# Kernel tuning notes

Hardware: AMD Instinct MI355X
Metric: run time of the kernel (lower is better)

## Reference

```python
import jax, jax.numpy as jnp
import numpy as np

B, S, D_IN, D_H, D_OUT = 4, 2048, 512, 512, 512


def setup_inputs() -> dict:
    key = jax.random.key(0)
    ks = jax.random.split(key, 11)
    s_in = 1.0 / np.sqrt(D_IN)
    s_cat = 1.0 / np.sqrt(3 * D_H)
    return {
        "x1": jax.random.normal(ks[0], (B, S, D_IN), jnp.float32),
        "x2": jax.random.normal(ks[1], (B, S, D_IN), jnp.float32),
        "x3": jax.random.normal(ks[2], (B, S, D_IN), jnp.float32),
        "Wq": jax.random.normal(ks[3], (D_IN, D_H), jnp.float32) * s_in,
        "bq": jnp.zeros((D_H,), jnp.float32),
        "Wk": jax.random.normal(ks[4], (D_IN, D_H), jnp.float32) * s_in,
        "bk": jnp.zeros((D_H,), jnp.float32),
        "Wv": jax.random.normal(ks[5], (D_IN, D_H), jnp.float32) * s_in,
        "bv": jnp.zeros((D_H,), jnp.float32),
        "Wo": jax.random.normal(ks[6], (3 * D_H, D_OUT), jnp.float32) * s_cat,
        "bo": jnp.zeros((D_OUT,), jnp.float32),
    }


def _attn(Q, K, V):
    # Q: [B,S,H], K/V: [B,S,H] -> [B,S,H]
    scale = 1.0 / jnp.sqrt(jnp.asarray(K.shape[-1], Q.dtype))
    scores = jnp.einsum('bqh,bkh->bqk', Q, K) * scale
    w = jax.nn.softmax(scores, axis=-1)
    return jnp.einsum('bqk,bkh->bqh', w, V)


def reference(x1, x2, x3, Wq, bq, Wk, bk, Wv, bv, Wo, bo):
    Q1, Q2, Q3 = x1 @ Wq + bq, x2 @ Wq + bq, x3 @ Wq + bq
    K1, K2, K3 = x1 @ Wk + bk, x2 @ Wk + bk, x3 @ Wk + bk
    V1, V2, V3 = x1 @ Wv + bv, x2 @ Wv + bv, x3 @ Wv + bv
    fused_x1 = _attn(Q1, K2, V2) + _attn(Q1, K3, V3)
    fused_x2 = _attn(Q2, K1, V1) + _attn(Q2, K3, V3)
    fused_x3 = _attn(Q3, K1, V1) + _attn(Q3, K2, V2)
    fused = jnp.concatenate([fused_x1, fused_x2, fused_x3], axis=-1)
    return fused @ Wo + bo
```

## Files before the change

kernel.cpp:

```cpp
#include <hip/hip_runtime.h>
#include <hip/hip_bf16.h>

typedef __attribute__((ext_vector_type(4))) float  f32x4;
typedef __attribute__((ext_vector_type(8))) short  short8;

#define GAS(p) ((const __attribute__((address_space(1))) void*)(p))
#define LAS(p) ((__attribute__((address_space(3))) void*)(p))

__device__ inline short bf16_of(float f) {
    union { float f; unsigned u; } v; v.f = f;
    unsigned r = v.u + 0x7FFFu + ((v.u >> 16) & 1u);
    return (short)(r >> 16);
}

__device__ __forceinline__ void stage64(const short* A, long lda,
                                        const short* B, long ldb,
                                        short* As, short* Bs) {
    const int tid = threadIdx.x;
    const int w = tid >> 6, l = tid & 63;
    const int r = l >> 3;
    const int scol = ((l & 7) ^ r) * 8;
#pragma unroll
    for (int q = 0; q < 4; ++q) {
        const int rowb = q * 32 + w * 8;
        __builtin_amdgcn_global_load_lds(GAS(A + (long)(rowb + r) * lda + scol),
                                         LAS(As + rowb * 64), 16, 0, 0);
        __builtin_amdgcn_global_load_lds(GAS(B + (long)(rowb + r) * ldb + scol),
                                         LAS(Bs + rowb * 64), 16, 0, 0);
    }
}

__device__ __forceinline__ void gemm_core64(const short* A, long lda,
                                            const short* B, long ldb, int nk,
                                            short* sA, short* sB,
                                            f32x4 acc[4][4]) {
    const int tid = threadIdx.x;
    const int lane = tid & 63, wid = tid >> 6;
    const int wr = wid >> 1, wc = wid & 1;
    const int fr = lane & 15, fk = lane >> 4;
    const int swz = (fr & 7) << 4;
    const int abase = (wr * 64 + fr) * 128 + fk * 16;
    const int bbase = (wc * 64 + fr) * 128 + fk * 16;

    stage64(A, lda, B, ldb, sA, sB);
    __syncthreads();
    for (int ks = 0; ks < nk; ++ks) {
        const int cur = ks & 1;
        if (ks + 1 < nk)
            stage64(A + (ks + 1) * 64, lda, B + (ks + 1) * 64, ldb,
                    sA + (cur ^ 1) * 8192, sB + (cur ^ 1) * 8192);
        const char* pa = (const char*)(sA + cur * 8192);
        const char* pb = (const char*)(sB + cur * 8192);
        short8 af[2][4], bfr[2][4];
#pragma unroll
        for (int kk = 0; kk < 2; ++kk) {
#pragma unroll
            for (int mi = 0; mi < 4; ++mi)
                af[kk][mi] = *(const short8*)(pa + (((abase + kk * 64) ^ swz) + mi * 2048));
#pragma unroll
            for (int ni = 0; ni < 4; ++ni)
                bfr[kk][ni] = *(const short8*)(pb + (((bbase + kk * 64) ^ swz) + ni * 2048));
        }
#pragma unroll
        for (int kk = 0; kk < 2; ++kk)
#pragma unroll
            for (int mi = 0; mi < 4; ++mi)
#pragma unroll
                for (int ni = 0; ni < 4; ++ni)
                    acc[mi][ni] = __builtin_amdgcn_mfma_f32_16x16x32_bf16(af[kk][mi], bfr[kk][ni], acc[mi][ni], 0, 0, 0);
        __syncthreads();
    }
}

__device__ __forceinline__ void bounce_store(short* Pb, const short vals[4][4][4],
                                             short* C, long ldc) {
    const int tid = threadIdx.x, lane = tid & 63, wid = tid >> 6;
    const int wr = wid >> 1, wc = wid & 1, fr = lane & 15, fk = lane >> 4;
#pragma unroll
    for (int mi = 0; mi < 4; ++mi)
#pragma unroll
        for (int ni = 0; ni < 4; ++ni)
#pragma unroll
            for (int r = 0; r < 4; ++r) {
                const int row = wr * 64 + mi * 16 + fk * 4 + r;
                const int col = wc * 64 + ni * 16 + fr;
                Pb[row * 128 + (col ^ ((row & 7) << 3))] = vals[mi][ni][r];
            }
    __syncthreads();
#pragma unroll
    for (int i = 0; i < 8; ++i) {
        const int row = i * 16 + (tid >> 4);
        const int ch = tid & 15;
        short8 v = *(const short8*)&Pb[row * 128 + ((ch * 8) ^ ((row & 7) << 3))];
        *(short8*)&C[(long)row * ldc + ch * 8] = v;
    }
}

__global__ __launch_bounds__(256, 2)
void proj_qk_k(const short* __restrict__ xb, const short* __restrict__ WqkT,
               short* __restrict__ Qb, short* __restrict__ Kb,
               const float* __restrict__ bq, const float* __restrict__ bk) {
    __shared__ short sA[2 * 8192], sB[2 * 8192];
    const short* Ab = xb + (long)blockIdx.x * 128 * 512;
    const short* Bb = WqkT + (long)blockIdx.y * 128 * 512;
    f32x4 acc[4][4] = {};
    gemm_core64(Ab, 512, Bb, 512, 8, sA, sB, acc);

    const int lane = threadIdx.x & 63, wid = threadIdx.x >> 6;
    const int wr = wid >> 1, wc = wid & 1, fr = lane & 15, fk = lane >> 4;
    const int qc0 = blockIdx.y * 128;
    const float* bias = qc0 < 512 ? bq + qc0 : bk + (qc0 - 512);
    short vals[4][4][4];
#pragma unroll
    for (int mi = 0; mi < 4; ++mi)
#pragma unroll
        for (int ni = 0; ni < 4; ++ni) {
            const float bv_ = bias[wc * 64 + ni * 16 + fr];
#pragma unroll
            for (int r = 0; r < 4; ++r)
                vals[mi][ni][r] = bf16_of(acc[mi][ni][r] + bv_);
        }
    short* dst = (qc0 < 512 ? Qb + qc0 : Kb + (qc0 - 512)) + (long)blockIdx.x * 128 * 512;
    bounce_store(sA, vals, dst, 512);
}

__global__ __launch_bounds__(256, 2)
void proj_vt_k(const short* __restrict__ WvT, const short* __restrict__ xb,
               short* __restrict__ VT, const float* __restrict__ bv) {
    __shared__ short sA[2 * 8192], sB[2 * 8192];
    const short* Ab = WvT + (long)blockIdx.x * 128 * 512;
    const short* Bb = xb + (long)blockIdx.y * 128 * 512;
    f32x4 acc[4][4] = {};
    gemm_core64(Ab, 512, Bb, 512, 8, sA, sB, acc);

    const int lane = threadIdx.x & 63, wid = threadIdx.x >> 6;
    const int wr = wid >> 1, wc = wid & 1, fr = lane & 15, fk = lane >> 4;
    short vals[4][4][4];
#pragma unroll
    for (int mi = 0; mi < 4; ++mi)
#pragma unroll
        for (int ni = 0; ni < 4; ++ni)
#pragma unroll
            for (int r = 0; r < 4; ++r) {
                const int rowg = blockIdx.x * 128 + wr * 64 + mi * 16 + fk * 4 + r;
                vals[mi][ni][r] = bf16_of(acc[mi][ni][r] + bv[rowg]);
            }
    bounce_store(sA, vals, VT + (long)blockIdx.x * 128 * 24576 + blockIdx.y * 128, 24576);
}

struct Off6 { long a[6], b[6]; };

__global__ __launch_bounds__(256, 2)
void qk_exp(const short* __restrict__ Qb, const short* __restrict__ Kb,
            short* __restrict__ Sc, float* __restrict__ lpart,
            Off6 o, int z0, float kscale) {
    __shared__ short sA[2 * 8192], sB[2 * 8192];
    const int z = blockIdx.z, slice = z0 + z;
    const int gp = slice >> 2, b = slice & 3;
    const short* Ab = Qb + o.a[gp] + ((long)b * 2048 + (long)blockIdx.x * 128) * 512;
    const short* Bb = Kb + o.b[gp] + ((long)b * 2048 + (long)blockIdx.y * 128) * 512;
    f32x4 acc[4][4] = {};
    gemm_core64(Ab, 512, Bb, 512, 8, sA, sB, acc);

    const int tid = threadIdx.x, lane = tid & 63, wid = tid >> 6;
    const int wr = wid >> 1, wc = wid & 1, fr = lane & 15, fk = lane >> 4;

#pragma unroll
    for (int mi = 0; mi < 4; ++mi)
#pragma unroll
        for (int ni = 0; ni < 4; ++ni)
#pragma unroll
            for (int r = 0; r < 4; ++r)
                acc[mi][ni][r] = exp2f(acc[mi][ni][r] * kscale);

#pragma unroll
    for (int mi = 0; mi < 4; ++mi)
#pragma unroll
        for (int r = 0; r < 4; ++r) {
            float s = acc[mi][0][r] + acc[mi][1][r] + acc[mi][2][r] + acc[mi][3][r];
            s += __shfl_xor(s, 1); s += __shfl_xor(s, 2);
            s += __shfl_xor(s, 4); s += __shfl_xor(s, 8);
            if (fr == 0)
                lpart[((long)z * 32 + blockIdx.y * 2 + wc) * 2048 +
                      (long)blockIdx.x * 128 + wr * 64 + mi * 16 + fk * 4 + r] = s;
        }

    short vals[4][4][4];
#pragma unroll
    for (int mi = 0; mi < 4; ++mi)
#pragma unroll
        for (int ni = 0; ni < 4; ++ni)
#pragma unroll
            for (int r = 0; r < 4; ++r)
                vals[mi][ni][r] = bf16_of(acc[mi][ni][r]);

    short* Cb = Sc + (long)z * 2048 * 2048 +
                (long)blockIdx.x * 128 * 2048 + (long)blockIdx.y * 128;
    bounce_store(sA, vals, Cb, 2048);
}

struct POff { long v[6], c[6]; };

__global__ __launch_bounds__(256, 2)
void pv_div(const short* __restrict__ Sc, const short* __restrict__ VT,
            const float* __restrict__ lpart, short* __restrict__ F,
            POff o, int z0) {
    __shared__ short sA[2 * 8192], sB[2 * 8192];
    const int z = blockIdx.z, slice = z0 + z;
    const int gp = slice >> 2, b = slice & 3;
    const short* Ab = Sc + (long)z * 2048 * 2048 + (long)blockIdx.x * 128 * 2048;
    const short* Bb = VT + o.v[gp] + (long)b * 2048 + (long)blockIdx.y * 128 * 24576;
    f32x4 acc[4][4] = {};
    gemm_core64(Ab, 2048, Bb, 24576, 32, sA, sB, acc);

    const int tid = threadIdx.x, lane = tid & 63, wid = tid >> 6;
    const int wr = wid >> 1, wc = wid & 1, fr = lane & 15, fk = lane >> 4;

    float* linv_s = (float*)sB;
    if (tid < 128) {
        const float* lp = lpart + ((long)z * 32) * 2048 + (long)blockIdx.x * 128 + tid;
        float s = 0.f;
#pragma unroll
        for (int j = 0; j < 32; ++j) s += lp[(long)j * 2048];
        linv_s[tid] = 1.0f / s;
    }
    __syncthreads();

    short vals[4][4][4];
#pragma unroll
    for (int mi = 0; mi < 4; ++mi) {
        float linv[4];
#pragma unroll
        for (int r = 0; r < 4; ++r) linv[r] = linv_s[wr * 64 + mi * 16 + fk * 4 + r];
#pragma unroll
        for (int ni = 0; ni < 4; ++ni)
#pragma unroll
            for (int r = 0; r < 4; ++r)
                vals[mi][ni][r] = bf16_of(acc[mi][ni][r] * linv[r]);
    }
    __syncthreads();

    short* Cb = F + ((long)b * 2048 + (long)blockIdx.x * 128) * 3072 +
                o.c[gp] + (long)blockIdx.y * 128;
    bounce_store(sA, vals, Cb, 3072);
}

__global__ __launch_bounds__(256, 2)
void final_f32(const short* __restrict__ A, const short* __restrict__ B,
               float* __restrict__ C, const float* __restrict__ bias) {
    __shared__ short sA[2 * 8192], sB[2 * 8192];
    const short* Ab = A + (long)blockIdx.x * 128 * 3072;
    const short* Bb = B + (long)blockIdx.y * 128 * 3072;
    f32x4 acc[4][4] = {};
    gemm_core64(Ab, 3072, Bb, 3072, 48, sA, sB, acc);

    const int lane = threadIdx.x & 63, wid = threadIdx.x >> 6;
    const int wr = wid >> 1, wc = wid & 1, fr = lane & 15, fk = lane >> 4;
    const long r0 = (long)blockIdx.x * 128 + wr * 64 + fk * 4;
    const long c0 = (long)blockIdx.y * 128 + wc * 64 + fr;
#pragma unroll
    for (int mi = 0; mi < 4; ++mi)
#pragma unroll
        for (int ni = 0; ni < 4; ++ni) {
            const long rr = r0 + mi * 16, cc = c0 + ni * 16;
#pragma unroll
            for (int r = 0; r < 4; ++r)
                C[(rr + r) * 512 + cc] = acc[mi][ni][r] + bias[cc];
        }
}

__global__ __launch_bounds__(256)
void xconv(const float* __restrict__ x0, const float* __restrict__ x1,
           const float* __restrict__ x2, short* __restrict__ xb) {
    const float* s = blockIdx.z == 0 ? x0 : (blockIdx.z == 1 ? x1 : x2);
    const long i = ((long)blockIdx.x * 256 + threadIdx.x) * 8;
    f32x4 a = *(const f32x4*)(s + i), c = *(const f32x4*)(s + i + 4);
    short8 v;
    v[0] = bf16_of(a.x); v[1] = bf16_of(a.y); v[2] = bf16_of(a.z); v[3] = bf16_of(a.w);
    v[4] = bf16_of(c.x); v[5] = bf16_of(c.y); v[6] = bf16_of(c.z); v[7] = bf16_of(c.w);
    *(short8*)(xb + (long)blockIdx.z * 8192 * 512 + i) = v;
}

__global__ __launch_bounds__(256)
void wprep(const float* __restrict__ Wq, const float* __restrict__ Wk,
           const float* __restrict__ Wv, const float* __restrict__ Wo,
           short* __restrict__ WqkT, short* __restrict__ WvT,
           short* __restrict__ WoT2) {
    __shared__ float t[32][33];
    const int z = blockIdx.z;
    const float* src; short* dst; int rows; long ldd; bool dup = false;
    if (z == 0)      { src = Wq; dst = WqkT;              rows = 512;  ldd = 512; }
    else if (z == 1) { src = Wk; dst = WqkT + 512L * 512; rows = 512;  ldd = 512; }
    else if (z == 2) { src = Wv; dst = WvT;               rows = 512;  ldd = 512; }
    else             { src = Wo; dst = WoT2;              rows = 1536; ldd = 3072; dup = true; }
    const int r0 = blockIdx.x * 32, c0 = blockIdx.y * 32;
    if (r0 >= rows) return;
    const int lx = threadIdx.x & 31, ly = threadIdx.x >> 5;
#pragma unroll
    for (int p = 0; p < 4; ++p)
        t[ly + 8 * p][lx] = src[(long)(r0 + ly + 8 * p) * 512 + (c0 + lx)];
    __syncthreads();
#pragma unroll
    for (int p = 0; p < 4; ++p) {
        const short v = bf16_of(t[lx][ly + 8 * p]);
        const long base = (long)(c0 + ly + 8 * p) * ldd + (r0 + lx);
        dst[base] = v;
        if (dup) dst[base + 1536] = v;
    }
}

extern "C" void kernel_launch(void* const* d_in, const int* in_sizes, int n_in,
                              void* d_out, int out_size, void* d_ws, size_t ws_size,
                              hipStream_t stream) {
    const float* x[3] = { (const float*)d_in[0], (const float*)d_in[1], (const float*)d_in[2] };
    const float* Wq = (const float*)d_in[3]; const float* bq = (const float*)d_in[4];
    const float* Wk = (const float*)d_in[5]; const float* bk = (const float*)d_in[6];
    const float* Wv = (const float*)d_in[7]; const float* bv = (const float*)d_in[8];
    const float* Wo = (const float*)d_in[9]; const float* bo = (const float*)d_in[10];

    const long TOK = 8192, T3 = 3 * TOK;

    char* ws = (char*)d_ws;
    size_t off = 0;
    auto alloc = [&](size_t bytes) -> void* {
        void* pp = ws + off;
        off += (bytes + 255) & ~(size_t)255;
        return pp;
    };

    short* WqkT  = (short*)alloc(1024L * 512 * 2);
    short* WvT   = (short*)alloc(512L * 512 * 2);
    short* WoT2  = (short*)alloc(512L * 3072 * 2);
    short* Qb    = (short*)alloc(T3 * 512 * 2);
    short* Kb    = (short*)alloc(T3 * 512 * 2);
    short* VT    = (short*)alloc(512L * T3 * 2);
    short* fused = (short*)alloc(TOK * 3072 * 2);
    float* lpart = (float*)alloc(8L * 32 * 2048 * 4);
    short* xb    = (short*)alloc(T3 * 512 * 2);

    const size_t SLICE = 2048L * 2048 * 2;
    const size_t rem = ws_size > off ? ws_size - off : 0;
    const int nsl = (rem >= 8 * SLICE) ? 8 : 4;
    short* scores = (short*)alloc((size_t)nsl * SLICE);

    const dim3 tb(256);
    wprep<<<dim3(48, 16, 4), tb, 0, stream>>>(Wq, Wk, Wv, Wo, WqkT, WvT, WoT2);
    xconv<<<dim3(2048, 1, 3), tb, 0, stream>>>(x[0], x[1], x[2], xb);

    proj_qk_k<<<dim3(192, 8), tb, 0, stream>>>(xb, WqkT, Qb, Kb, bq, bk);
    proj_vt_k<<<dim3(4, 192), tb, 0, stream>>>(WvT, xb, VT, bv);

    const int imap[6] = {0, 1, 2, 0, 1, 2};
    const int jmap[6] = {1, 0, 0, 2, 2, 1};
    Off6 qo{}; POff po{};
    for (int gp = 0; gp < 6; ++gp) {
        qo.a[gp] = (long)imap[gp] * TOK * 512;
        qo.b[gp] = (long)jmap[gp] * TOK * 512;
        po.v[gp] = (long)jmap[gp] * TOK;
        po.c[gp] = (long)imap[gp] * 512 + (gp >= 3 ? 1536 : 0);
    }
    const float kscale = 0.04419417382415922f * 1.4426950408889634f;

    for (int z0 = 0; z0 < 24; z0 += nsl) {
        qk_exp<<<dim3(16, 16, nsl), tb, 0, stream>>>(Qb, Kb, scores, lpart, qo, z0, kscale);
        pv_div<<<dim3(16, 4, nsl), tb, 0, stream>>>(scores, VT, lpart, fused, po, z0);
    }

    final_f32<<<dim3(64, 4), tb, 0, stream>>>(fused, WoT2, (float*)d_out, bo);
}
```

Before: 441.4 us.

## Fuse QK-exp and PV passes into a single flash-style attention kernel

Replaces the two-kernel attention (QK^T with exp written to a bf16 score buffer in global memory, then a PV GEMM with normalization) with one fused kernel. Each block handles 32 query rows across all 2048 keys, keeping probabilities in LDS and accumulating PV directly. The goal is to stop writing and re-reading the large score matrices and to cut the per-chunk launch loop. Operands are read straight from global memory with no LDS staging or double buffering, and K/V are reloaded for every 32-row query block, so memory traffic and latency could become the new bottleneck.

```diff
diff --git a/kernel.cpp b/kernel.cpp
--- a/kernel.cpp
+++ b/kernel.cpp
@@ -12,6 +12,8 @@
     unsigned r = v.u + 0x7FFFu + ((v.u >> 16) & 1u);
     return (short)(r >> 16);
 }
+
+#define MFMA __builtin_amdgcn_mfma_f32_16x16x32_bf16
 
 __device__ __forceinline__ void stage64(const short* A, long lda,
                                         const short* B, long ldb,
@@ -67,7 +69,7 @@
             for (int mi = 0; mi < 4; ++mi)
 #pragma unroll
                 for (int ni = 0; ni < 4; ++ni)
-                    acc[mi][ni] = __builtin_amdgcn_mfma_f32_16x16x32_bf16(af[kk][mi], bfr[kk][ni], acc[mi][ni], 0, 0, 0);
+                    acc[mi][ni] = MFMA(af[kk][mi], bfr[kk][ni], acc[mi][ni], 0, 0, 0);
         __syncthreads();
     }
 }
@@ -107,7 +109,7 @@
     gemm_core64(Ab, 512, Bb, 512, 8, sA, sB, acc);
 
     const int lane = threadIdx.x & 63, wid = threadIdx.x >> 6;
-    const int wr = wid >> 1, wc = wid & 1, fr = lane & 15, fk = lane >> 4;
+    const int wc = wid & 1, fr = lane & 15;
     const int qc0 = blockIdx.y * 128;
     const float* bias = qc0 < 512 ? bq + qc0 : bk + (qc0 - 512);
     short vals[4][4][4];
@@ -134,7 +136,7 @@
     gemm_core64(Ab, 512, Bb, 512, 8, sA, sB, acc);
 
     const int lane = threadIdx.x & 63, wid = threadIdx.x >> 6;
-    const int wr = wid >> 1, wc = wid & 1, fr = lane & 15, fk = lane >> 4;
+    const int wr = wid >> 1, fk = lane >> 4;
     short vals[4][4][4];
 #pragma unroll
     for (int mi = 0; mi < 4; ++mi)
@@ -148,101 +150,131 @@
     bounce_store(sA, vals, VT + (long)blockIdx.x * 128 * 24576 + blockIdx.y * 128, 24576);
 }
 
-struct Off6 { long a[6], b[6]; };
-
-__global__ __launch_bounds__(256, 2)
-void qk_exp(const short* __restrict__ Qb, const short* __restrict__ Kb,
-            short* __restrict__ Sc, float* __restrict__ lpart,
-            Off6 o, int z0, float kscale) {
-    __shared__ short sA[2 * 8192], sB[2 * 8192];
-    const int z = blockIdx.z, slice = z0 + z;
+struct FOff { long q[6], k[6], v[6], c[6]; };
+
+__global__ __launch_bounds__(512, 4)
+void fattn(const short* __restrict__ Qb, const short* __restrict__ Kb,
+           const short* __restrict__ VT, short* __restrict__ F,
+           FOff fo, float kscale) {
+    __shared__ short Pb[32 * 256];
+    __shared__ short Ob[16 * 512];
+    const int tid = threadIdx.x;
+    const int w = tid >> 6, lane = tid & 63;
+    const int fr = lane & 15, fk = lane >> 4;
+    const int slice = blockIdx.z;
     const int gp = slice >> 2, b = slice & 3;
-    const short* Ab = Qb + o.a[gp] + ((long)b * 2048 + (long)blockIdx.x * 128) * 512;
-    const short* Bb = Kb + o.b[gp] + ((long)b * 2048 + (long)blockIdx.y * 128) * 512;
-    f32x4 acc[4][4] = {};
-    gemm_core64(Ab, 512, Bb, 512, 8, sA, sB, acc);
-
-    const int tid = threadIdx.x, lane = tid & 63, wid = tid >> 6;
-    const int wr = wid >> 1, wc = wid & 1, fr = lane & 15, fk = lane >> 4;
-
-#pragma unroll
-    for (int mi = 0; mi < 4; ++mi)
-#pragma unroll
-        for (int ni = 0; ni < 4; ++ni)
+
+    const short* Qp = Qb + fo.q[gp] + ((long)b * 2048 + (long)blockIdx.x * 32) * 512;
+    const short* Kp = Kb + fo.k[gp] + ((long)b * 2048 + w * 32 + fr) * 512;
+    const short* Vp = VT + fo.v[gp] + (long)b * 2048 + ((long)w * 64 + fr) * 24576;
+
+    const short* qa0 = Qp + (long)fr * 512;
+    const short* qa1 = Qp + (long)(16 + fr) * 512;
+
+    f32x4 ov[2][4] = {};
+    float lrow[2][4] = {};
+    const int prow0 = fk * 4;
+
+#pragma unroll 1
+    for (int kt = 0; kt < 8; ++kt) {
+        f32x4 s[2][2] = {{{}, {}}, {{}, {}}};
+        const short* kp0 = Kp + (long)kt * 256 * 512;
+        const short* kp1 = kp0 + 16 * 512;
+#pragma unroll
+        for (int ks = 0; ks < 16; ++ks) {
+            const int off = ks * 32 + fk * 8;
+            short8 b0 = *(const short8*)(kp0 + off);
+            short8 b1 = *(const short8*)(kp1 + off);
+            short8 a0 = *(const short8*)(qa0 + off);
+            short8 a1 = *(const short8*)(qa1 + off);
+            s[0][0] = MFMA(a0, b0, s[0][0], 0, 0, 0);
+            s[0][1] = MFMA(a0, b1, s[0][1], 0, 0, 0);
+            s[1][0] = MFMA(a1, b0, s[1][0], 0, 0, 0);
+            s[1][1] = MFMA(a1, b1, s[1][1], 0, 0, 0);
+        }
+        __syncthreads();
+#pragma unroll
+        for (int m = 0; m < 2; ++m)
+#pragma unroll
+            for (int n = 0; n < 2; ++n)
+#pragma unroll
+                for (int r = 0; r < 4; ++r) {
+                    float p = exp2f(s[m][n][r] * kscale);
+                    lrow[m][r] += p;
+                    const int row = m * 16 + prow0 + r;
+                    const int col = w * 32 + n * 16 + fr;
+                    Pb[row * 256 + (col ^ ((row & 7) << 3))] = bf16_of(p);
+                }
+        __syncthreads();
+#pragma unroll
+        for (int ks = 0; ks < 8; ++ks) {
+            const int chunk = ks * 4 + fk;
+            const int r0 = fr, r1 = 16 + fr;
+            short8 pa0 = *(const short8*)((const char*)Pb + r0 * 512 + ((chunk ^ (r0 & 7)) * 16));
+            short8 pa1 = *(const short8*)((const char*)Pb + r1 * 512 + ((chunk ^ (r1 & 7)) * 16));
+            const int voff = kt * 256 + ks * 32 + fk * 8;
+#pragma unroll
+            for (int n = 0; n < 4; ++n) {
+                short8 vf = *(const short8*)(Vp + (long)n * 16 * 24576 + voff);
+                ov[0][n] = MFMA(pa0, vf, ov[0][n], 0, 0, 0);
+                ov[1][n] = MFMA(pa1, vf, ov[1][n], 0, 0, 0);
+            }
+        }
+    }
+
+    __syncthreads();
+    float* Lred = (float*)Pb;
+#pragma unroll
+    for (int m = 0; m < 2; ++m)
+#pragma unroll
+        for (int r = 0; r < 4; ++r) {
+            float v = lrow[m][r];
+            v += __shfl_xor(v, 1); v += __shfl_xor(v, 2);
+            v += __shfl_xor(v, 4); v += __shfl_xor(v, 8);
+            lrow[m][r] = v;
+        }
+    if (fr == 0) {
+#pragma unroll
+        for (int m = 0; m < 2; ++m)
 #pragma unroll
             for (int r = 0; r < 4; ++r)
-                acc[mi][ni][r] = exp2f(acc[mi][ni][r] * kscale);
-
-#pragma unroll
-    for (int mi = 0; mi < 4; ++mi)
+                Lred[w * 32 + m * 16 + prow0 + r] = lrow[m][r];
+    }
+    __syncthreads();
+    float linv[2][4];
+#pragma unroll
+    for (int m = 0; m < 2; ++m)
 #pragma unroll
         for (int r = 0; r < 4; ++r) {
-            float s = acc[mi][0][r] + acc[mi][1][r] + acc[mi][2][r] + acc[mi][3][r];
-            s += __shfl_xor(s, 1); s += __shfl_xor(s, 2);
-            s += __shfl_xor(s, 4); s += __shfl_xor(s, 8);
-            if (fr == 0)
-                lpart[((long)z * 32 + blockIdx.y * 2 + wc) * 2048 +
-                      (long)blockIdx.x * 128 + wr * 64 + mi * 16 + fk * 4 + r] = s;
-        }
-
-    short vals[4][4][4];
-#pragma unroll
-    for (int mi = 0; mi < 4; ++mi)
-#pragma unroll
-        for (int ni = 0; ni < 4; ++ni)
-#pragma unroll
-            for (int r = 0; r < 4; ++r)
-                vals[mi][ni][r] = bf16_of(acc[mi][ni][r]);
-
-    short* Cb = Sc + (long)z * 2048 * 2048 +
-                (long)blockIdx.x * 128 * 2048 + (long)blockIdx.y * 128;
-    bounce_store(sA, vals, Cb, 2048);
-}
-
-struct POff { long v[6], c[6]; };
-
-__global__ __launch_bounds__(256, 2)
-void pv_div(const short* __restrict__ Sc, const short* __restrict__ VT,
-            const float* __restrict__ lpart, short* __restrict__ F,
-            POff o, int z0) {
-    __shared__ short sA[2 * 8192], sB[2 * 8192];
-    const int z = blockIdx.z, slice = z0 + z;
-    const int gp = slice >> 2, b = slice & 3;
-    const short* Ab = Sc + (long)z * 2048 * 2048 + (long)blockIdx.x * 128 * 2048;
-    const short* Bb = VT + o.v[gp] + (long)b * 2048 + (long)blockIdx.y * 128 * 24576;
-    f32x4 acc[4][4] = {};
-    gemm_core64(Ab, 2048, Bb, 24576, 32, sA, sB, acc);
-
-    const int tid = threadIdx.x, lane = tid & 63, wid = tid >> 6;
-    const int wr = wid >> 1, wc = wid & 1, fr = lane & 15, fk = lane >> 4;
-
-    float* linv_s = (float*)sB;
-    if (tid < 128) {
-        const float* lp = lpart + ((long)z * 32) * 2048 + (long)blockIdx.x * 128 + tid;
-        float s = 0.f;
-#pragma unroll
-        for (int j = 0; j < 32; ++j) s += lp[(long)j * 2048];
-        linv_s[tid] = 1.0f / s;
-    }
-    __syncthreads();
-
-    short vals[4][4][4];
-#pragma unroll
-    for (int mi = 0; mi < 4; ++mi) {
-        float linv[4];
-#pragma unroll
-        for (int r = 0; r < 4; ++r) linv[r] = linv_s[wr * 64 + mi * 16 + fk * 4 + r];
-#pragma unroll
-        for (int ni = 0; ni < 4; ++ni)
-#pragma unroll
-            for (int r = 0; r < 4; ++r)
-                vals[mi][ni][r] = bf16_of(acc[mi][ni][r] * linv[r]);
-    }
-    __syncthreads();
-
-    short* Cb = F + ((long)b * 2048 + (long)blockIdx.x * 128) * 3072 +
-                o.c[gp] + (long)blockIdx.y * 128;
-    bounce_store(sA, vals, Cb, 3072);
+            const int row = m * 16 + prow0 + r;
+            float sum = 0.f;
+#pragma unroll
+            for (int w8 = 0; w8 < 8; ++w8) sum += Lred[w8 * 32 + row];
+            linv[m][r] = 1.0f / sum;
+        }
+
+    const long c0 = fo.c[gp];
+    const long orow = (long)b * 2048 + (long)blockIdx.x * 32;
+#pragma unroll
+    for (int m = 0; m < 2; ++m) {
+        __syncthreads();
+#pragma unroll
+        for (int n = 0; n < 4; ++n)
+#pragma unroll
+            for (int r = 0; r < 4; ++r) {
+                const int row = prow0 + r;
+                const int col = w * 64 + n * 16 + fr;
+                Ob[row * 512 + (col ^ ((row & 7) << 3))] = bf16_of(ov[m][n][r] * linv[m][r]);
+            }
+        __syncthreads();
+#pragma unroll
+        for (int sp = 0; sp < 2; ++sp) {
+            const int row = sp * 8 + (tid >> 6);
+            const int ch = tid & 63;
+            short8 v8 = *(const short8*)&Ob[row * 512 + ((ch ^ (row & 7)) * 8)];
+            *(short8*)&F[(orow + m * 16 + row) * 3072 + c0 + ch * 8] = v8;
+        }
+    }
 }
 
 __global__ __launch_bounds__(256, 2)
@@ -335,13 +367,7 @@
     short* Kb    = (short*)alloc(T3 * 512 * 2);
     short* VT    = (short*)alloc(512L * T3 * 2);
     short* fused = (short*)alloc(TOK * 3072 * 2);
-    float* lpart = (float*)alloc(8L * 32 * 2048 * 4);
     short* xb    = (short*)alloc(T3 * 512 * 2);
-
-    const size_t SLICE = 2048L * 2048 * 2;
-    const size_t rem = ws_size > off ? ws_size - off : 0;
-    const int nsl = (rem >= 8 * SLICE) ? 8 : 4;
-    short* scores = (short*)alloc((size_t)nsl * SLICE);
 
     const dim3 tb(256);
     wprep<<<dim3(48, 16, 4), tb, 0, stream>>>(Wq, Wk, Wv, Wo, WqkT, WvT, WoT2);
@@ -352,19 +378,16 @@
 
     const int imap[6] = {0, 1, 2, 0, 1, 2};
     const int jmap[6] = {1, 0, 0, 2, 2, 1};
-    Off6 qo{}; POff po{};
+    FOff fo{};
     for (int gp = 0; gp < 6; ++gp) {
-        qo.a[gp] = (long)imap[gp] * TOK * 512;
-        qo.b[gp] = (long)jmap[gp] * TOK * 512;
-        po.v[gp] = (long)jmap[gp] * TOK;
-        po.c[gp] = (long)imap[gp] * 512 + (gp >= 3 ? 1536 : 0);
+        fo.q[gp] = (long)imap[gp] * TOK * 512;
+        fo.k[gp] = (long)jmap[gp] * TOK * 512;
+        fo.v[gp] = (long)jmap[gp] * TOK;
+        fo.c[gp] = (long)imap[gp] * 512 + (gp >= 3 ? 1536 : 0);
     }
     const float kscale = 0.04419417382415922f * 1.4426950408889634f;
 
-    for (int z0 = 0; z0 < 24; z0 += nsl) {
-        qk_exp<<<dim3(16, 16, nsl), tb, 0, stream>>>(Qb, Kb, scores, lpart, qo, z0, kscale);
-        pv_div<<<dim3(16, 4, nsl), tb, 0, stream>>>(scores, VT, lpart, fused, po, z0);
-    }
+    fattn<<<dim3(64, 1, 24), dim3(512), 0, stream>>>(Qb, Kb, VT, fused, fo, kscale);
 
     final_f32<<<dim3(64, 4), tb, 0, stream>>>(fused, WoT2, (float*)d_out, bo);
 }
```

After: 1.183 ms. 2.68x slower.

## Keep Q tile in registers and stream four K tiles per qk_exp block

Applied to the files above, without the earlier changes.

The QK^T + exp kernel now loads each wave's 32 query rows into registers once and streams K through double-buffered LDS, with each block computing four 128-wide score tiles instead of one. Row-sum partials drop from 32 to 4 per row, so pv_div reduces fewer partials. This is meant to cut redundant Q loads and LDS staging of the A operand, and to reduce launch count and lpart traffic. In exchange it uses many more registers (qreg holds 32 short8 values) and a single-stage prefetch pipeline with fewer blocks, which could lower occupancy and parallelism.

```diff
diff --git a/kernel.cpp b/kernel.cpp
--- a/kernel.cpp
+++ b/kernel.cpp
@@ -12,6 +12,8 @@
     unsigned r = v.u + 0x7FFFu + ((v.u >> 16) & 1u);
     return (short)(r >> 16);
 }
+
+#define MFMA __builtin_amdgcn_mfma_f32_16x16x32_bf16
 
 __device__ __forceinline__ void stage64(const short* A, long lda,
                                         const short* B, long ldb,
@@ -67,7 +69,7 @@
             for (int mi = 0; mi < 4; ++mi)
 #pragma unroll
                 for (int ni = 0; ni < 4; ++ni)
-                    acc[mi][ni] = __builtin_amdgcn_mfma_f32_16x16x32_bf16(af[kk][mi], bfr[kk][ni], acc[mi][ni], 0, 0, 0);
+                    acc[mi][ni] = MFMA(af[kk][mi], bfr[kk][ni], acc[mi][ni], 0, 0, 0);
         __syncthreads();
     }
 }
@@ -107,7 +109,7 @@
     gemm_core64(Ab, 512, Bb, 512, 8, sA, sB, acc);
 
     const int lane = threadIdx.x & 63, wid = threadIdx.x >> 6;
-    const int wr = wid >> 1, wc = wid & 1, fr = lane & 15, fk = lane >> 4;
+    const int wc = wid & 1, fr = lane & 15;
     const int qc0 = blockIdx.y * 128;
     const float* bias = qc0 < 512 ? bq + qc0 : bk + (qc0 - 512);
     short vals[4][4][4];
@@ -134,7 +136,7 @@
     gemm_core64(Ab, 512, Bb, 512, 8, sA, sB, acc);
 
     const int lane = threadIdx.x & 63, wid = threadIdx.x >> 6;
-    const int wr = wid >> 1, wc = wid & 1, fr = lane & 15, fk = lane >> 4;
+    const int wr = wid >> 1, fk = lane >> 4;
     short vals[4][4][4];
 #pragma unroll
     for (int mi = 0; mi < 4; ++mi)
@@ -154,49 +156,107 @@
 void qk_exp(const short* __restrict__ Qb, const short* __restrict__ Kb,
             short* __restrict__ Sc, float* __restrict__ lpart,
             Off6 o, int z0, float kscale) {
-    __shared__ short sA[2 * 8192], sB[2 * 8192];
+    __shared__ short sB[2 * 8192];
+    __shared__ short Pb[128 * 128];
     const int z = blockIdx.z, slice = z0 + z;
     const int gp = slice >> 2, b = slice & 3;
-    const short* Ab = Qb + o.a[gp] + ((long)b * 2048 + (long)blockIdx.x * 128) * 512;
-    const short* Bb = Kb + o.b[gp] + ((long)b * 2048 + (long)blockIdx.y * 128) * 512;
-    f32x4 acc[4][4] = {};
-    gemm_core64(Ab, 512, Bb, 512, 8, sA, sB, acc);
-
-    const int tid = threadIdx.x, lane = tid & 63, wid = tid >> 6;
-    const int wr = wid >> 1, wc = wid & 1, fr = lane & 15, fk = lane >> 4;
-
-#pragma unroll
-    for (int mi = 0; mi < 4; ++mi)
-#pragma unroll
-        for (int ni = 0; ni < 4; ++ni)
-#pragma unroll
-            for (int r = 0; r < 4; ++r)
-                acc[mi][ni][r] = exp2f(acc[mi][ni][r] * kscale);
-
-#pragma unroll
-    for (int mi = 0; mi < 4; ++mi)
+    const int tid = threadIdx.x, lane = tid & 63, w = tid >> 6;
+    const int fr = lane & 15, fk = lane >> 4;
+
+    const short* Qp = Qb + o.a[gp] + ((long)b * 2048 + blockIdx.x * 128 + w * 32) * 512;
+    const short* Kp = Kb + o.b[gp] + ((long)b * 2048 + blockIdx.y * 512) * 512;
+
+    short8 qreg[2][16];
+#pragma unroll
+    for (int mi = 0; mi < 2; ++mi)
+#pragma unroll
+        for (int c = 0; c < 16; ++c)
+            qreg[mi][c] = *(const short8*)(Qp + (long)(mi * 16 + fr) * 512 + c * 32 + fk * 8);
+
+    const int sr = lane >> 3;
+    const int scol = ((lane & 7) ^ sr) * 8;
+    const int swz = (fr & 7) << 4;
+
+    auto stageB = [&](int t) {
+        const short* src = Kp + (long)(t >> 3) * 128 * 512 + (t & 7) * 64;
+        short* dst = sB + (t & 1) * 8192;
+#pragma unroll
+        for (int q = 0; q < 4; ++q) {
+            const int rowb = q * 32 + w * 8;
+            __builtin_amdgcn_global_load_lds(GAS(src + (long)(rowb + sr) * 512 + scol),
+                                             LAS(dst + rowb * 64), 16, 0, 0);
+        }
+    };
+
+    float lrow[2][4] = {};
+    f32x4 acc[2][8] = {};
+
+    stageB(0);
+    __syncthreads();
+
+#pragma unroll 1
+    for (int t = 0; t < 32; ++t) {
+        if (t + 1 < 32) stageB(t + 1);
+        const char* pb = (const char*)(sB + (t & 1) * 8192);
+        const int ks = t & 7;
+#pragma unroll
+        for (int kk = 0; kk < 2; ++kk) {
+            const int c = ks * 2 + kk;
+            short8 bf[8];
+#pragma unroll
+            for (int ni = 0; ni < 8; ++ni)
+                bf[ni] = *(const short8*)(pb + ((((ni * 16 + fr) * 128 + fk * 16) + kk * 64) ^ swz));
+#pragma unroll
+            for (int ni = 0; ni < 8; ++ni) {
+                acc[0][ni] = MFMA(qreg[0][c], bf[ni], acc[0][ni], 0, 0, 0);
+                acc[1][ni] = MFMA(qreg[1][c], bf[ni], acc[1][ni], 0, 0, 0);
+            }
+        }
+        __syncthreads();
+
+        if ((t & 7) == 7) {
+            const int yy = t >> 3;
+#pragma unroll
+            for (int mi = 0; mi < 2; ++mi)
+#pragma unroll
+                for (int ni = 0; ni < 8; ++ni)
+#pragma unroll
+                    for (int r = 0; r < 4; ++r) {
+                        float p = exp2f(acc[mi][ni][r] * kscale);
+                        lrow[mi][r] += p;
+                        const int row = w * 32 + mi * 16 + fk * 4 + r;
+                        const int col = ni * 16 + fr;
+                        Pb[row * 128 + (col ^ ((row & 7) << 3))] = bf16_of(p);
+                    }
+            __syncthreads();
+            short* Cb = Sc + (long)z * 2048 * 2048 + (long)blockIdx.x * 128 * 2048 +
+                        (blockIdx.y * 4 + yy) * 128;
+#pragma unroll
+            for (int i = 0; i < 8; ++i) {
+                const int row = i * 16 + (tid >> 4);
+                const int ch = tid & 15;
+                short8 v = *(const short8*)&Pb[row * 128 + ((ch * 8) ^ ((row & 7) << 3))];
+                *(short8*)&Cb[(long)row * 2048 + ch * 8] = v;
+            }
+#pragma unroll
+            for (int mi = 0; mi < 2; ++mi)
+#pragma unroll
+                for (int ni = 0; ni < 8; ++ni)
+                    acc[mi][ni] = f32x4{0.f, 0.f, 0.f, 0.f};
+        }
+    }
+
+#pragma unroll
+    for (int mi = 0; mi < 2; ++mi)
 #pragma unroll
         for (int r = 0; r < 4; ++r) {
-            float s = acc[mi][0][r] + acc[mi][1][r] + acc[mi][2][r] + acc[mi][3][r];
-            s += __shfl_xor(s, 1); s += __shfl_xor(s, 2);
-            s += __shfl_xor(s, 4); s += __shfl_xor(s, 8);
+            float v = lrow[mi][r];
+            v += __shfl_xor(v, 1); v += __shfl_xor(v, 2);
+            v += __shfl_xor(v, 4); v += __shfl_xor(v, 8);
             if (fr == 0)
-                lpart[((long)z * 32 + blockIdx.y * 2 + wc) * 2048 +
-                      (long)blockIdx.x * 128 + wr * 64 + mi * 16 + fk * 4 + r] = s;
-        }
-
-    short vals[4][4][4];
-#pragma unroll
-    for (int mi = 0; mi < 4; ++mi)
-#pragma unroll
-        for (int ni = 0; ni < 4; ++ni)
-#pragma unroll
-            for (int r = 0; r < 4; ++r)
-                vals[mi][ni][r] = bf16_of(acc[mi][ni][r]);
-
-    short* Cb = Sc + (long)z * 2048 * 2048 +
-                (long)blockIdx.x * 128 * 2048 + (long)blockIdx.y * 128;
-    bounce_store(sA, vals, Cb, 2048);
+                lpart[((long)z * 4 + blockIdx.y) * 2048 +
+                      (long)blockIdx.x * 128 + w * 32 + mi * 16 + fk * 4 + r] = v;
+        }
 }
 
 struct POff { long v[6], c[6]; };
@@ -218,11 +278,8 @@
 
     float* linv_s = (float*)sB;
     if (tid < 128) {
-        const float* lp = lpart + ((long)z * 32) * 2048 + (long)blockIdx.x * 128 + tid;
-        float s = 0.f;
-#pragma unroll
-        for (int j = 0; j < 32; ++j) s += lp[(long)j * 2048];
-        linv_s[tid] = 1.0f / s;
+        const float* lp = lpart + (long)z * 4 * 2048 + (long)blockIdx.x * 128 + tid;
+        linv_s[tid] = 1.0f / (lp[0] + lp[2048] + lp[4096] + lp[6144]);
     }
     __syncthreads();
 
@@ -335,7 +392,7 @@
     short* Kb    = (short*)alloc(T3 * 512 * 2);
     short* VT    = (short*)alloc(512L * T3 * 2);
     short* fused = (short*)alloc(TOK * 3072 * 2);
-    float* lpart = (float*)alloc(8L * 32 * 2048 * 4);
+    float* lpart = (float*)alloc(8L * 4 * 2048 * 4);
     short* xb    = (short*)alloc(T3 * 512 * 2);
 
     const size_t SLICE = 2048L * 2048 * 2;
@@ -362,7 +419,7 @@
     const float kscale = 0.04419417382415922f * 1.4426950408889634f;
 
     for (int z0 = 0; z0 < 24; z0 += nsl) {
-        qk_exp<<<dim3(16, 16, nsl), tb, 0, stream>>>(Qb, Kb, scores, lpart, qo, z0, kscale);
+        qk_exp<<<dim3(16, 4, nsl), tb, 0, stream>>>(Qb, Kb, scores, lpart, qo, z0, kscale);
         pv_div<<<dim3(16, 4, nsl), tb, 0, stream>>>(scores, VT, lpart, fused, po, z0);
     }
 
```

Measured after the change: 573.4 us. 1.3x slower.
